# Kernel tuning notes

Hardware: AMD Instinct MI355X
Metric: run time of the kernel (lower is better)

The kernel has to match this reference:

```python
import jax, jax.numpy as jnp
import numpy as np

BS, D, N, E, L, NE = 8, 512, 2048, 8, 64, 524288


def conv1d_same(x, w, b):
    # x: [B, W, Cin], w: [K, Cin, Cout] -> [B, W, Cout], stride 1, 'same' padding
    y = jax.lax.conv_general_dilated(x, w, window_strides=(1,), padding='SAME',
                                     dimension_numbers=('NWC', 'WIO', 'NWC'))
    return y + b


def setup_inputs() -> dict:
    key = jax.random.key(0)
    ks = jax.random.split(key, 10)
    def nrm(k, shape, s=1.0):
        return jax.random.normal(k, shape, jnp.float32) * s
    return {
        'latent': nrm(ks[0], (BS, D)),
        'edge_index': jax.random.randint(ks[1], (2, NE), 0, BS * N),
        'W_dense': nrm(ks[2], (D, N), 0.05),
        'b_dense': jnp.zeros((N,), jnp.float32),
        'conv1_w': nrm(ks[3], (3, 1, E), 0.3),
        'conv1_b': jnp.zeros((E,), jnp.float32),
        'gat_Wq': nrm(ks[4], (E, E), 0.3),
        'gat_bq': jnp.zeros((E,), jnp.float32),
        'gat_Wk': nrm(ks[5], (E, E), 0.3),
        'gat_bk': jnp.zeros((E,), jnp.float32),
        'gat_Wv': nrm(ks[6], (E, E), 0.3),
        'gat_bias': jnp.zeros((E,), jnp.float32),
        'qkv_w': nrm(ks[7], (3, E, 3 * E * L), 0.1),
        'qkv_b': jnp.zeros((3 * E * L,), jnp.float32),
    }


def reference(latent, edge_index, W_dense, b_dense, conv1_w, conv1_b,
              gat_Wq, gat_bq, gat_Wk, gat_bk, gat_Wv, gat_bias, qkv_w, qkv_b):
    bs = latent.shape[0]
    # Dense -> [bs, N], expand -> Conv1D(E) -> [bs, N, E]
    skeleton = latent @ W_dense + b_dense
    skeleton = conv1d_same(skeleton[..., None], conv1_w, conv1_b)
    # concat(unstack, axis=0) == reshape to batched graph nodes [bs*N, E]
    x = skeleton.reshape(bs * N, E)
    BN = bs * N
    # GAT (tf_geometric, num_heads=1): add self-loops, per-edge dot-attention,
    # segment softmax over destination (row), scatter-sum aggregate.
    loops = jnp.arange(BN)
    row = jnp.concatenate([edge_index[0], loops])
    col = jnp.concatenate([edge_index[1], loops])
    Q = jax.nn.leaky_relu(x @ gat_Wq + gat_bq, 0.2)
    K = jax.nn.leaky_relu(x @ gat_Wk + gat_bk, 0.2)
    V = x @ gat_Wv
    score = jnp.sum(Q[row] * K[col], axis=-1)            # [n_edges + BN]
    smax = jax.ops.segment_max(score, row, num_segments=BN)
    ex = jnp.exp(score - smax[row])
    ssum = jax.ops.segment_sum(ex, row, num_segments=BN)
    alpha = ex / ssum[row]                               # segment softmax
    h = jax.ops.segment_sum(alpha[:, None] * V[col], row, num_segments=BN) + gat_bias
    graph = h.reshape(bs, N, E)                          # stack(split(., bs))
    # QVK conv over node axis -> [bs, N, 3*E*L]
    qvk = conv1d_same(graph, qkv_w, qkv_b)
    # stack(split(., L, -1), 1) then concat(unstack(., -2), -1)
    qvk = qvk.reshape(bs, N, L, 3 * E).transpose(0, 2, 1, 3).reshape(bs, L, N * 3 * E)
    q, v, k = jnp.split(qvk, 3, axis=-1)                 # each [bs, L, N*E]
    # keras Attention (use_scale=False): softmax(q @ k^T) @ v
    attn = jax.nn.softmax(jnp.einsum('btd,bsd->bts', q, k), axis=-1)
    seq = jnp.einsum('bts,bsd->btd', attn, v)
    # stack(split(., N, -1), -2) == reshape [bs, L, N, E]
    return seq.reshape(bs, L, N, E)
```

## Files before the change

### kernel.cpp

```cpp
#include <hip/hip_runtime.h>
#include <hip/hip_bf16.h>
#include <math.h>

#define BSZ 8
#define DDIM 512
#define NND 2048
#define EE 8
#define LLH 64
#define NEDGE 524288
#define BNN 16384
#define OCC 1536
#define DQ 16384
#define NCHK 22

typedef __attribute__((ext_vector_type(8))) short short8;
typedef __attribute__((ext_vector_type(4))) float f32x4;

__device__ inline unsigned short f2bf(float x) {
    __hip_bfloat16 h = __float2bfloat16(x);
    return __builtin_bit_cast(unsigned short, h);
}
__device__ inline float bf2f(unsigned short u) {
    return __uint_as_float(((unsigned int)u) << 16);
}

__global__ __launch_bounds__(256) void k_densep(const float* __restrict__ latent,
                                                const float* __restrict__ Wd,
                                                float* __restrict__ pdense) {
    int n0 = blockIdx.x * 32, d0 = blockIdx.y * 64;
    __shared__ float lat[8][64];
    int tid = threadIdx.x;
    #pragma unroll
    for (int r = 0; r < 2; ++r) {
        int i = r * 256 + tid;
        lat[i >> 6][i & 63] = latent[(i >> 6) * DDIM + d0 + (i & 63)];
    }
    __syncthreads();
    int nl = tid & 31, b = tid >> 5;
    const float* wp = Wd + (size_t)d0 * NND + n0 + nl;
    float acc = 0.f;
    #pragma unroll 8
    for (int d = 0; d < 64; ++d) acc += lat[b][d] * wp[(size_t)d * NND];
    pdense[((size_t)blockIdx.y * BSZ + b) * NND + n0 + nl] = acc;
}

__global__ __launch_bounds__(64) void k_gat(const float* __restrict__ pdense,
                                            const float* __restrict__ bd,
                                            const float* __restrict__ w1,
                                            const float* __restrict__ b1,
                                            const float* __restrict__ Wq, const float* __restrict__ bq,
                                            const float* __restrict__ Wk, const float* __restrict__ bk,
                                            const float* __restrict__ Wv,
                                            float* __restrict__ Qg, float* __restrict__ Kg,
                                            float* __restrict__ Vg, int* __restrict__ hist) {
    int i = blockIdx.x * 64 + threadIdx.x;
    int b = i >> 11, n = i & (NND - 1);
    float sm = 0.f, s0 = 0.f, sp = 0.f;
    #pragma unroll
    for (int ds = 0; ds < 8; ++ds) {
        const float* p = pdense + ((size_t)ds * BSZ + b) * NND + n;
        if (n > 0) sm += p[-1];
        s0 += p[0];
        if (n < NND - 1) sp += p[1];
    }
    if (n > 0) sm += bd[n - 1];
    s0 += bd[n];
    if (n < NND - 1) sp += bd[n + 1];
    float xr[EE];
    #pragma unroll
    for (int e = 0; e < EE; ++e)
        xr[e] = sm * w1[e] + s0 * w1[EE + e] + sp * w1[2 * EE + e] + b1[e];
    #pragma unroll
    for (int j = 0; j < EE; ++j) {
        float q = bq[j], k = bk[j], v = 0.f;
        #pragma unroll
        for (int c = 0; c < EE; ++c) {
            q += xr[c] * Wq[c * EE + j];
            k += xr[c] * Wk[c * EE + j];
            v += xr[c] * Wv[c * EE + j];
        }
        Qg[(size_t)i * EE + j] = (q >= 0.f) ? q : 0.2f * q;
        Kg[(size_t)i * EE + j] = (k >= 0.f) ? k : 0.2f * k;
        Vg[(size_t)i * EE + j] = v;
    }
    hist[i] = 0;
}

__global__ void k_hist(const int* __restrict__ ei, int* __restrict__ hist) {
    int e = blockIdx.x * 256 + threadIdx.x;
    if (e >= NEDGE) return;
    atomicAdd(hist + ei[e], 1);
}

__global__ __launch_bounds__(256) void k_scan(const int* __restrict__ hist,
                                              int* __restrict__ offs,
                                              int* __restrict__ cnt) {
    __shared__ int part[256];
    int tid = threadIdx.x;
    int base = tid * 64;
    const int4* h4 = (const int4*)(hist + base);
    int sum = 0;
    #pragma unroll
    for (int i = 0; i < 16; ++i) { int4 v = h4[i]; sum += v.x + v.y + v.z + v.w; }
    part[tid] = sum;
    __syncthreads();
    for (int off = 1; off < 256; off <<= 1) {
        int v = (tid >= off) ? part[tid - off] : 0;
        __syncthreads();
        part[tid] += v;
        __syncthreads();
    }
    int run = (tid > 0) ? part[tid - 1] : 0;
    for (int i = 0; i < 64; ++i) {
        offs[base + i] = run;
        cnt[base + i] = run;
        run += hist[base + i];
    }
}

__global__ void k_scatter(const int* __restrict__ ei, int* __restrict__ cnt,
                          int* __restrict__ ecol) {
    int e = blockIdx.x * 256 + threadIdx.x;
    if (e >= NEDGE) return;
    int r = ei[e], c = ei[NEDGE + e];
    int pos = atomicAdd(cnt + r, 1);
    ecol[pos] = c;
}

__global__ __launch_bounds__(256) void k_gatagg(const int* __restrict__ ecol,
                                                const int* __restrict__ offs,
                                                const int* __restrict__ hist,
                                                const float* __restrict__ Qg,
                                                const float* __restrict__ Kg,
                                                const float* __restrict__ Vg,
                                                const float* __restrict__ gbias,
                                                float* __restrict__ hg) {
    int row = __builtin_amdgcn_readfirstlane(blockIdx.x * 4 + (threadIdx.x >> 6));
    int lane = threadIdx.x & 63;
    const float* Qr = Qg + (size_t)row * EE;
    float q0 = Qr[0], q1 = Qr[1], q2 = Qr[2], q3 = Qr[3];
    float q4 = Qr[4], q5 = Qr[5], q6 = Qr[6], q7 = Qr[7];
    int beg = offs[row], deg = hist[row];
    int total = deg + 1;
    float m = -INFINITY, l = 0.f;
    float acc[EE];
    #pragma unroll
    for (int j = 0; j < EE; ++j) acc[j] = 0.f;
    for (int base = 0; base < total; base += 64) {
        int idx = base + lane;
        int c = row;
        if (idx < deg) c = ecol[beg + idx];
        const float4* K4 = (const float4*)(Kg + (size_t)c * EE);
        float4 ka = K4[0], kb = K4[1];
        float s = q0*ka.x + q1*ka.y + q2*ka.z + q3*ka.w
                + q4*kb.x + q5*kb.y + q6*kb.z + q7*kb.w;
        if (idx >= total) s = -INFINITY;
        float pm = s;
        #pragma unroll
        for (int off = 32; off > 0; off >>= 1) pm = fmaxf(pm, __shfl_xor(pm, off));
        float nm = fmaxf(m, pm);
        float scale = __expf(m - nm);
        float p = (idx < total) ? __expf(s - nm) : 0.f;
        float ps = p;
        #pragma unroll
        for (int off = 32; off > 0; off >>= 1) ps += __shfl_xor(ps, off);
        l = l * scale + ps;
        const float4* V4 = (const float4*)(Vg + (size_t)c * EE);
        float4 va = V4[0], vb = V4[1];
        float pv[EE] = {p*va.x, p*va.y, p*va.z, p*va.w, p*vb.x, p*vb.y, p*vb.z, p*vb.w};
        #pragma unroll
        for (int j = 0; j < EE; ++j) {
            float t = pv[j];
            #pragma unroll
            for (int off = 32; off > 0; off >>= 1) t += __shfl_xor(t, off);
            acc[j] = acc[j] * scale + t;
        }
        m = nm;
    }
    if (lane < EE)
        hg[(size_t)row * EE + lane] = acc[lane] / l + gbias[lane];
}

__global__ __launch_bounds__(256) void k_qkvF(const float* __restrict__ hg,
                                              const float* __restrict__ qw,
                                              const float* __restrict__ qb,
                                              unsigned short* __restrict__ Fq) {
    int n0 = blockIdx.x * 32;
    int b = blockIdx.y;
    __shared__ float hs[34 * EE];
    int tid = threadIdx.x;
    for (int i = tid; i < 34 * EE; i += 256) {
        int nn = n0 - 1 + (i >> 3);
        hs[i] = (nn >= 0 && nn < NND) ? hg[((size_t)b * NND + nn) * EE + (i & 7)] : 0.f;
    }
    __syncthreads();
    #pragma unroll
    for (int pass = 0; pass < 2; ++pass) {
        float w[3][24], bias[3];
        #pragma unroll
        for (int rr = 0; rr < 3; ++rr) {
            int o = tid + (pass * 3 + rr) * 256;
            bias[rr] = qb[o];
            #pragma unroll
            for (int kk = 0; kk < 24; ++kk) w[rr][kk] = qw[kk * OCC + o];
        }
        for (int nn = 0; nn < 32; ++nn) {
            const float* hv = &hs[nn * EE];
            float a0 = bias[0], a1 = bias[1], a2 = bias[2];
            #pragma unroll
            for (int kk = 0; kk < 24; ++kk) {
                float h = hv[kk];
                a0 += h * w[0][kk]; a1 += h * w[1][kk]; a2 += h * w[2][kk];
            }
            unsigned short* dst = Fq + ((size_t)b * NND + n0 + nn) * OCC + tid + pass * 768;
            dst[0]   = f2bf(a0);
            dst[256] = f2bf(a1);
            dst[512] = f2bf(a2);
        }
    }
}

__global__ __launch_bounds__(256) void k_attnS(const unsigned short* __restrict__ Fq,
                                               float* __restrict__ Spart) {
    int ch = blockIdx.x, b = blockIdx.y;
    __shared__ unsigned short qt[64 * 200];
    __shared__ unsigned short kt[64 * 200];
    int tid = threadIdx.x;
    int t = tid & 63, nl0 = tid >> 6;
    const unsigned short* Fb = Fq + (size_t)b * NND * OCC;
    short8 z = {0,0,0,0,0,0,0,0};
    int lane = tid & 63, wv = tid >> 6;
    int fr = lane & 15, fk = (lane >> 4) * 8;
    f32x4 accs[4] = {{0,0,0,0},{0,0,0,0},{0,0,0,0},{0,0,0,0}};
    for (int sub = 0; sub < 4; ++sub) {
        int n0 = ch * 32 + sub * 8;
        if (sub) __syncthreads();
        #pragma unroll
        for (int h = 0; h < 2; ++h) {
            int nl = nl0 + h * 4;
            int n = n0 + nl;
            short8 q0 = z, q1 = z, q2 = z;
            if (n <= 682) {
                const short8* p = (const short8*)(Fb + (size_t)n * OCC + t * 24);
                q0 = p[0]; q1 = p[1];
                if (n < 682) q2 = p[2];
            }
            *(short8*)(&qt[t * 200 + nl * 24 + 0])  = q0;
            *(short8*)(&qt[t * 200 + nl * 24 + 8])  = q1;
            *(short8*)(&qt[t * 200 + nl * 24 + 16]) = q2;
            short8 k0 = z, k1 = z, k2 = z;
            if (n <= 682) {
                const short8* p = (const short8*)(Fb + (size_t)(n + 1365) * OCC + t * 24 + 8);
                k0 = p[0]; k1 = p[1];
            }
            if (n <= 681) {
                const short8* p2 = (const short8*)(Fb + (size_t)(n + 1366) * OCC + t * 24);
                k2 = p2[0];
            }
            *(short8*)(&kt[t * 200 + nl * 24 + 0])  = k0;
            *(short8*)(&kt[t * 200 + nl * 24 + 8])  = k1;
            *(short8*)(&kt[t * 200 + nl * 24 + 16]) = k2;
        }
        __syncthreads();
        short8 afr[6];
        #pragma unroll
        for (int ks = 0; ks < 6; ++ks)
            afr[ks] = *(const short8*)(&qt[(wv * 16 + fr) * 200 + ks * 32 + fk]);
        #pragma unroll
        for (int srow = 0; srow < 4; ++srow) {
            #pragma unroll
            for (int ks = 0; ks < 6; ++ks) {
                short8 bfr = *(const short8*)(&kt[(srow * 16 + fr) * 200 + ks * 32 + fk]);
                accs[srow] = __builtin_amdgcn_mfma_f32_16x16x32_bf16(afr[ks], bfr, accs[srow], 0, 0, 0);
            }
        }
    }
    #pragma unroll
    for (int srow = 0; srow < 4; ++srow) {
        float* dst = Spart + (((size_t)ch * BSZ + b) * LLH + wv * 16 + (lane >> 4) * 4) * LLH
                   + srow * 16 + fr;
        #pragma unroll
        for (int r = 0; r < 4; ++r) dst[r * LLH] = accs[srow][r];
    }
}

__global__ void k_softmax(const float* __restrict__ Spart, float* __restrict__ atT) {
    int b = blockIdx.x >> 6, t = blockIdx.x & 63;
    int s = threadIdx.x;
    float v = 0.f;
    for (int ch = 0; ch < NCHK; ++ch)
        v += Spart[(((size_t)ch * BSZ + b) * LLH + t) * LLH + s];
    float m = v;
    #pragma unroll
    for (int off = 32; off > 0; off >>= 1) m = fmaxf(m, __shfl_xor(m, off));
    float e = __expf(v - m);
    float sum = e;
    #pragma unroll
    for (int off = 32; off > 0; off >>= 1) sum += __shfl_xor(sum, off);
    atT[((size_t)b * LLH + s) * LLH + t] = e / sum;
}

__global__ __launch_bounds__(256) void k_attnV(const unsigned short* __restrict__ Fq,
                                               const float* __restrict__ atT,
                                               float* __restrict__ out) {
    int b = blockIdx.y;
    int d = blockIdx.x * 64 + (threadIdx.x & 63);
    int t0 = __builtin_amdgcn_readfirstlane((threadIdx.x >> 6) * 16);
    int f = d + DQ;
    int n = f / 24, c = f - n * 24;
    const unsigned short* vcol = Fq + ((size_t)b * NND + n) * OCC + c;
    const float* arow = atT + (size_t)b * LLH * LLH + t0;
    float acc[16];
    #pragma unroll
    for (int tt = 0; tt < 16; ++tt) acc[tt] = 0.f;
    #pragma unroll 4
    for (int s = 0; s < LLH; ++s) {
        float vv = bf2f(vcol[s * 24]);
        #pragma unroll
        for (int tt = 0; tt < 16; ++tt)
            acc[tt] += arow[s * LLH + tt] * vv;
    }
    float* ob = out + ((size_t)b * LLH + t0) * DQ + d;
    #pragma unroll
    for (int tt = 0; tt < 16; ++tt) ob[(size_t)tt * DQ] = acc[tt];
}

extern "C" void kernel_launch(void* const* d_in, const int* in_sizes, int n_in,
                              void* d_out, int out_size, void* d_ws, size_t ws_size,
                              hipStream_t stream) {
    (void)in_sizes; (void)n_in; (void)out_size; (void)ws_size;
    const float* latent = (const float*)d_in[0];
    const int*   ei     = (const int*)d_in[1];
    const float* Wd     = (const float*)d_in[2];
    const float* bd     = (const float*)d_in[3];
    const float* w1     = (const float*)d_in[4];
    const float* b1     = (const float*)d_in[5];
    const float* Wq     = (const float*)d_in[6];
    const float* bq     = (const float*)d_in[7];
    const float* Wk     = (const float*)d_in[8];
    const float* bk     = (const float*)d_in[9];
    const float* Wv     = (const float*)d_in[10];
    const float* gbias  = (const float*)d_in[11];
    const float* qw     = (const float*)d_in[12];
    const float* qb     = (const float*)d_in[13];
    float* out = (float*)d_out;

    float* ws     = (float*)d_ws;
    float* pdense = ws;
    float* Qg     = pdense + 64 * NND;
    float* Kg     = Qg + BNN * EE;
    float* Vg     = Kg + BNN * EE;
    float* hg     = Vg + BNN * EE;
    int*   hist   = (int*)(hg + BNN * EE);
    int*   offs   = hist + BNN;
    int*   cnt    = offs + BNN;
    int*   ecol   = cnt + BNN;
    float* Spart  = (float*)(ecol + NEDGE);
    float* atT    = Spart + (size_t)NCHK * BSZ * LLH * LLH;
    unsigned short* Fq = (unsigned short*)(atT + BSZ * LLH * LLH);

    k_densep<<<dim3(64, 8), dim3(256), 0, stream>>>(latent, Wd, pdense);
    k_gat<<<dim3(256), dim3(64), 0, stream>>>(pdense, bd, w1, b1, Wq, bq, Wk, bk, Wv,
                                              Qg, Kg, Vg, hist);
    k_hist<<<dim3(NEDGE / 256), dim3(256), 0, stream>>>(ei, hist);
    k_scan<<<dim3(1), dim3(256), 0, stream>>>(hist, offs, cnt);
    k_scatter<<<dim3(NEDGE / 256), dim3(256), 0, stream>>>(ei, cnt, ecol);
    k_gatagg<<<dim3(BNN / 4), dim3(256), 0, stream>>>(ecol, offs, hist,
                                                      Qg, Kg, Vg, gbias, hg);
    k_qkvF<<<dim3(64, 8), dim3(256), 0, stream>>>(hg, qw, qb, Fq);
    k_attnS<<<dim3(NCHK, 8), dim3(256), 0, stream>>>(Fq, Spart);
    k_softmax<<<dim3(512), dim3(64), 0, stream>>>(Spart, atT);
    k_attnV<<<dim3(256, 8), dim3(256), 0, stream>>>(Fq, atT, out);
}
```

Before: 146.6 us.

## Fuse histogram into GAT kernel, wave-scan offsets, stage qkv and V tiles in LDS

Moves zeroing of the degree histogram into the dense kernel and folds the edge histogram atomics into the GAT projection kernel, which removes one launch. The single-block scan is rewritten for 1024 threads using wave shuffles instead of a barrier-heavy shared-memory loop. The qkv conv kernel now stages its bf16 outputs in LDS and writes them out as coalesced 16-byte vector stores. The attention-V kernel first gathers its strided V column tile into LDS. The cost is more LDS use per block and extra barriers.

```diff
diff --git a/kernel.cpp b/kernel.cpp
--- a/kernel.cpp
+++ b/kernel.cpp
@@ -26,10 +26,12 @@
 
 __global__ __launch_bounds__(256) void k_densep(const float* __restrict__ latent,
                                                 const float* __restrict__ Wd,
-                                                float* __restrict__ pdense) {
+                                                float* __restrict__ pdense,
+                                                int* __restrict__ hist) {
     int n0 = blockIdx.x * 32, d0 = blockIdx.y * 64;
     __shared__ float lat[8][64];
     int tid = threadIdx.x;
+    if (blockIdx.y == 0) hist[blockIdx.x * 256 + tid] = 0;
     #pragma unroll
     for (int r = 0; r < 2; ++r) {
         int i = r * 256 + tid;
@@ -51,6 +53,7 @@
                                             const float* __restrict__ Wq, const float* __restrict__ bq,
                                             const float* __restrict__ Wk, const float* __restrict__ bk,
                                             const float* __restrict__ Wv,
+                                            const int* __restrict__ ei,
                                             float* __restrict__ Qg, float* __restrict__ Kg,
                                             float* __restrict__ Vg, int* __restrict__ hist) {
     int i = blockIdx.x * 64 + threadIdx.x;
@@ -83,38 +86,48 @@
         Kg[(size_t)i * EE + j] = (k >= 0.f) ? k : 0.2f * k;
         Vg[(size_t)i * EE + j] = v;
     }
-    hist[i] = 0;
-}
-
-__global__ void k_hist(const int* __restrict__ ei, int* __restrict__ hist) {
-    int e = blockIdx.x * 256 + threadIdx.x;
-    if (e >= NEDGE) return;
-    atomicAdd(hist + ei[e], 1);
-}
-
-__global__ __launch_bounds__(256) void k_scan(const int* __restrict__ hist,
-                                              int* __restrict__ offs,
-                                              int* __restrict__ cnt) {
-    __shared__ int part[256];
+    #pragma unroll 4
+    for (int j = 0; j < 32; ++j)
+        atomicAdd(hist + ei[i + j * BNN], 1);
+}
+
+__global__ __launch_bounds__(1024) void k_scan(const int* __restrict__ hist,
+                                               int* __restrict__ offs,
+                                               int* __restrict__ cnt) {
     int tid = threadIdx.x;
-    int base = tid * 64;
-    const int4* h4 = (const int4*)(hist + base);
-    int sum = 0;
-    #pragma unroll
-    for (int i = 0; i < 16; ++i) { int4 v = h4[i]; sum += v.x + v.y + v.z + v.w; }
-    part[tid] = sum;
+    int lane = tid & 63, wv = tid >> 6;
+    const int4* hp = (const int4*)(hist + tid * 16);
+    int4 a = hp[0], b4 = hp[1], c4 = hp[2], d4 = hp[3];
+    int h[16] = {a.x, a.y, a.z, a.w, b4.x, b4.y, b4.z, b4.w,
+                 c4.x, c4.y, c4.z, c4.w, d4.x, d4.y, d4.z, d4.w};
+    int mysum = 0;
+    #pragma unroll
+    for (int i = 0; i < 16; ++i) mysum += h[i];
+    int inc = mysum;
+    #pragma unroll
+    for (int off = 1; off < 64; off <<= 1) {
+        int u = __shfl_up(inc, off, 64);
+        if (lane >= off) inc += u;
+    }
+    __shared__ int wtot[16];
+    if (lane == 63) wtot[wv] = inc;
     __syncthreads();
-    for (int off = 1; off < 256; off <<= 1) {
-        int v = (tid >= off) ? part[tid - off] : 0;
-        __syncthreads();
-        part[tid] += v;
-        __syncthreads();
-    }
-    int run = (tid > 0) ? part[tid - 1] : 0;
-    for (int i = 0; i < 64; ++i) {
-        offs[base + i] = run;
-        cnt[base + i] = run;
-        run += hist[base + i];
+    if (tid < 16) {
+        int t = wtot[tid];
+        #pragma unroll
+        for (int off = 1; off < 16; off <<= 1) {
+            int u = __shfl_up(t, off, 16);
+            if (tid >= off) t += u;
+        }
+        wtot[tid] = t;
+    }
+    __syncthreads();
+    int run = (wv ? wtot[wv - 1] : 0) + inc - mysum;
+    #pragma unroll
+    for (int i = 0; i < 16; ++i) {
+        offs[tid * 16 + i] = run;
+        cnt[tid * 16 + i] = run;
+        run += h[i];
     }
 }
 
@@ -188,6 +201,7 @@
     int n0 = blockIdx.x * 32;
     int b = blockIdx.y;
     __shared__ float hs[34 * EE];
+    __shared__ unsigned short st[32 * 768];
     int tid = threadIdx.x;
     for (int i = tid; i < 34 * EE; i += 256) {
         int nn = n0 - 1 + (i >> 3);
@@ -196,10 +210,11 @@
     __syncthreads();
     #pragma unroll
     for (int pass = 0; pass < 2; ++pass) {
+        if (pass) __syncthreads();
         float w[3][24], bias[3];
         #pragma unroll
         for (int rr = 0; rr < 3; ++rr) {
-            int o = tid + (pass * 3 + rr) * 256;
+            int o = pass * 768 + rr * 256 + tid;
             bias[rr] = qb[o];
             #pragma unroll
             for (int kk = 0; kk < 24; ++kk) w[rr][kk] = qw[kk * OCC + o];
@@ -212,10 +227,18 @@
                 float h = hv[kk];
                 a0 += h * w[0][kk]; a1 += h * w[1][kk]; a2 += h * w[2][kk];
             }
-            unsigned short* dst = Fq + ((size_t)b * NND + n0 + nn) * OCC + tid + pass * 768;
-            dst[0]   = f2bf(a0);
-            dst[256] = f2bf(a1);
-            dst[512] = f2bf(a2);
+            st[nn * 768 + tid]       = f2bf(a0);
+            st[nn * 768 + tid + 256] = f2bf(a1);
+            st[nn * 768 + tid + 512] = f2bf(a2);
+        }
+        __syncthreads();
+        unsigned short* dstbase = Fq + ((size_t)b * NND + n0) * OCC + pass * 768;
+        #pragma unroll
+        for (int it = 0; it < 12; ++it) {
+            int idx8 = it * 256 + tid;
+            int row = idx8 / 96, col8 = idx8 - row * 96;
+            *(short8*)(dstbase + (size_t)row * OCC + col8 * 8) =
+                *(const short8*)(&st[row * 768 + col8 * 8]);
         }
     }
 }
@@ -304,23 +327,33 @@
                                                const float* __restrict__ atT,
                                                float* __restrict__ out) {
     int b = blockIdx.y;
-    int d = blockIdx.x * 64 + (threadIdx.x & 63);
-    int t0 = __builtin_amdgcn_readfirstlane((threadIdx.x >> 6) * 16);
-    int f = d + DQ;
-    int n = f / 24, c = f - n * 24;
-    const unsigned short* vcol = Fq + ((size_t)b * NND + n) * OCC + c;
+    int d0 = blockIdx.x * 64;
+    int tid = threadIdx.x;
+    __shared__ unsigned short vt[64 * 64];
+    const unsigned short* Fb = Fq + (size_t)b * NND * OCC;
+    #pragma unroll
+    for (int r = 0; r < 16; ++r) {
+        int idx = r * 256 + tid;
+        int s = idx >> 6, d = idx & 63;
+        int f = DQ + d0 + d;
+        int n = f / 24, c = f - n * 24;
+        vt[s * 64 + d] = Fb[(size_t)n * OCC + s * 24 + c];
+    }
+    __syncthreads();
+    int lane = tid & 63;
+    int t0 = __builtin_amdgcn_readfirstlane((tid >> 6) * 16);
     const float* arow = atT + (size_t)b * LLH * LLH + t0;
     float acc[16];
     #pragma unroll
     for (int tt = 0; tt < 16; ++tt) acc[tt] = 0.f;
     #pragma unroll 4
     for (int s = 0; s < LLH; ++s) {
-        float vv = bf2f(vcol[s * 24]);
+        float vv = bf2f(vt[s * 64 + lane]);
         #pragma unroll
         for (int tt = 0; tt < 16; ++tt)
             acc[tt] += arow[s * LLH + tt] * vv;
     }
-    float* ob = out + ((size_t)b * LLH + t0) * DQ + d;
+    float* ob = out + ((size_t)b * LLH + t0) * DQ + d0 + lane;
     #pragma unroll
     for (int tt = 0; tt < 16; ++tt) ob[(size_t)tt * DQ] = acc[tt];
 }
@@ -359,11 +392,10 @@
     float* atT    = Spart + (size_t)NCHK * BSZ * LLH * LLH;
     unsigned short* Fq = (unsigned short*)(atT + BSZ * LLH * LLH);
 
-    k_densep<<<dim3(64, 8), dim3(256), 0, stream>>>(latent, Wd, pdense);
+    k_densep<<<dim3(64, 8), dim3(256), 0, stream>>>(latent, Wd, pdense, hist);
     k_gat<<<dim3(256), dim3(64), 0, stream>>>(pdense, bd, w1, b1, Wq, bq, Wk, bk, Wv,
-                                              Qg, Kg, Vg, hist);
-    k_hist<<<dim3(NEDGE / 256), dim3(256), 0, stream>>>(ei, hist);
-    k_scan<<<dim3(1), dim3(256), 0, stream>>>(hist, offs, cnt);
+                                              ei, Qg, Kg, Vg, hist);
+    k_scan<<<dim3(1), dim3(1024), 0, stream>>>(hist, offs, cnt);
     k_scatter<<<dim3(NEDGE / 256), dim3(256), 0, stream>>>(ei, cnt, ecol);
     k_gatagg<<<dim3(BNN / 4), dim3(256), 0, stream>>>(ecol, offs, hist,
                                                       Qg, Kg, Vg, gbias, hg);
```

Result: faster. 142.0 us (-3.1%).
